# Performance work log

Measured on AMD Instinct MI355X. Metric: run time of the kernel, lower is better.

The kernel has to match this reference:

```python
import jax, jax.numpy as jnp
import numpy as np
from jax import lax

A_RATIOS = (0.5, 1.0, 2.0)
A_SCALES = (8, 16, 32)
FEAT_STRIDE = 16
BASE_SIZE = 16
PRE_NMS = 6000     # n_test_pre_nms
POST_NMS = 300     # n_test_post_nms
NMS_THRESH = 0.7
MIN_SIZE = 16.0
SCALE = 1.0        # forward(scale=1.0) default
NEG = -1e10


def _anchor_base():
    # standard generate_anchor_base: centered at (8,8), ratios x scales
    py = px = BASE_SIZE / 2.0
    rows = []
    for r in A_RATIOS:
        for s in A_SCALES:
            h = BASE_SIZE * s * np.sqrt(r)
            w = BASE_SIZE * s * np.sqrt(1.0 / r)
            rows.append([py - h / 2.0, px - w / 2.0, py + h / 2.0, px + w / 2.0])
    return np.asarray(rows, np.float32)  # (A, 4)


def _all_anchors(height, width):
    base = jnp.asarray(_anchor_base())                                  # (A, 4)
    sy = (jnp.arange(height) * FEAT_STRIDE).astype(jnp.float32)
    sx = (jnp.arange(width) * FEAT_STRIDE).astype(jnp.float32)
    gy, gx = jnp.meshgrid(sy, sx, indexing='ij')
    shift = jnp.stack([gy.ravel(), gx.ravel(), gy.ravel(), gx.ravel()], axis=1)  # (K, 4)
    anch = base[None, :, :] + shift[:, None, :]                         # (K, A, 4)
    return anch.reshape(-1, 4)                                          # (K*A, 4)


def _conv(x, w, b, pad):
    y = lax.conv_general_dilated(x, w, (1, 1), [(pad, pad), (pad, pad)],
                                 dimension_numbers=('NCHW', 'OIHW', 'NCHW'))
    return y + b[None, :, None, None]


def _loc2bbox(anchors, locs):
    h = anchors[:, 2] - anchors[:, 0]
    w = anchors[:, 3] - anchors[:, 1]
    cy = anchors[:, 0] + 0.5 * h
    cx = anchors[:, 1] + 0.5 * w
    dy, dx, dh, dw = locs[:, 0], locs[:, 1], locs[:, 2], locs[:, 3]
    ncy = dy * h + cy
    ncx = dx * w + cx
    nh = jnp.exp(dh) * h
    nw = jnp.exp(dw) * w
    return jnp.stack([ncy - 0.5 * nh, ncx - 0.5 * nw,
                      ncy + 0.5 * nh, ncx + 0.5 * nw], axis=1)


def _iou_one_vs_all(box, boxes):
    ty = jnp.maximum(box[0], boxes[:, 0])
    tx = jnp.maximum(box[1], boxes[:, 1])
    by = jnp.minimum(box[2], boxes[:, 2])
    bx = jnp.minimum(box[3], boxes[:, 3])
    inter = jnp.maximum(by - ty, 0.0) * jnp.maximum(bx - tx, 0.0)
    a1 = (box[2] - box[0]) * (box[3] - box[1])
    a2 = (boxes[:, 2] - boxes[:, 0]) * (boxes[:, 3] - boxes[:, 1])
    return inter / (a1 + a2 - inter + 1e-9)


def _nms(boxes, scores):
    # greedy NMS with fixed POST_NMS output; invalid slots are zero boxes
    def step(s, _):
        i = jnp.argmax(s)
        valid = s[i] > NEG / 2
        ious = _iou_one_vs_all(boxes[i], boxes)
        s = jnp.where(ious > NMS_THRESH, NEG, s)  # suppresses self (iou=1)
        return s, (i, valid)
    _, (idx, valid) = lax.scan(step, scores, None, length=POST_NMS)
    return boxes[idx] * valid[:, None].astype(boxes.dtype)  # (POST_NMS, 4)


def _proposals(anchors, locs, fg, img_h, img_w):
    boxes = _loc2bbox(anchors, locs)
    boxes = jnp.stack([jnp.clip(boxes[:, 0], 0.0, img_h),
                       jnp.clip(boxes[:, 1], 0.0, img_w),
                       jnp.clip(boxes[:, 2], 0.0, img_h),
                       jnp.clip(boxes[:, 3], 0.0, img_w)], axis=1)
    hs = boxes[:, 2] - boxes[:, 0]
    ws = boxes[:, 3] - boxes[:, 1]
    ok = (hs >= MIN_SIZE * SCALE) & (ws >= MIN_SIZE * SCALE)
    sc = jnp.where(ok, fg, NEG)
    top_sc, idx = lax.top_k(sc, PRE_NMS)
    return _nms(boxes[idx], top_sc)


def reference(base_feat, W_conv1, b_conv1, W_score, b_score, W_loc, b_loc, img_h, img_w):
    N, _, H, W = base_feat.shape
    A = 9
    mid = jax.nn.relu(_conv(base_feat, W_conv1, b_conv1, 1))            # (N,512,H,W)
    rpn_locs = _conv(mid, W_loc, b_loc, 0).transpose(0, 2, 3, 1).reshape(N, H * W * A, 4)
    raw = _conv(mid, W_score, b_score, 0).transpose(0, 2, 3, 1)          # (N,H,W,2A)
    rpn_scores = raw.reshape(N, H * W * A, 2)
    fg = jax.nn.softmax(raw.reshape(N, H, W, A, 2), axis=-1)[..., 1].reshape(N, -1)
    anchors = _all_anchors(H, W)                                         # (H*W*A,4)
    ih, iw = float(img_h), float(img_w)
    prop = jax.vmap(lambda l, f: _proposals(anchors, l, f, ih, iw))(rpn_locs, fg)
    rois = prop.reshape(N * POST_NMS, 4)
    roi_indices = jnp.repeat(jnp.arange(N, dtype=jnp.int32), POST_NMS)
    return rpn_locs, rpn_scores, rois, roi_indices, anchors


def setup_inputs() -> dict:
    key = jax.random.key(0)
    k0, k1, k2, k3 = jax.random.split(key, 4)
    N, C, H, W = 4, 512, 64, 64
    nA = 9
    return {
        'base_feat': jax.random.normal(k0, (N, C, H, W), jnp.float32),
        'W_conv1': 0.01 * jax.random.normal(k1, (512, 512, 3, 3), jnp.float32),
        'b_conv1': jnp.zeros((512,), jnp.float32),
        'W_score': 0.01 * jax.random.normal(k2, (2 * nA, 512, 1, 1), jnp.float32),
        'b_score': jnp.zeros((2 * nA,), jnp.float32),
        'W_loc': 0.01 * jax.random.normal(k3, (4 * nA, 512, 1, 1), jnp.float32),
        'b_loc': jnp.zeros((4 * nA,), jnp.float32),
        'img_h': 1024,
        'img_w': 1024,
    }
```

## Files before the change

### kernel.cpp

```cpp
#include <hip/hip_runtime.h>
#include <math.h>

#define HH 64
#define WW 64
#define NIMG 4
#define CIN 512
#define AA 9
#define HWA (HH*WW*AA)
#define PRE_NMS 6000
#define POST_NMS 300
#define NEGV (-1e10f)
#define NEGK 0xD01502F9u
#define NWORD 94

#define OFF1 589824
#define OFF2 884736
#define OFF3 889536
#define OFF4 890736

typedef unsigned int u32;
typedef unsigned long long u64;
typedef _Float16 f16;
typedef _Float16 half8 __attribute__((ext_vector_type(8)));
typedef float f32x4 __attribute__((ext_vector_type(4)));

__device__ __forceinline__ void gload_lds16(const void* g, void* l)
{
    __builtin_amdgcn_global_load_lds((const __attribute__((address_space(1))) void*)g,
                                     (__attribute__((address_space(3))) void*)l,
                                     16, 0, 0);
}

__global__ __launch_bounds__(256) void k_prep_x(const float* __restrict__ x,
                                                f16* __restrict__ xh,
                                                f16* __restrict__ xl)
{
    __shared__ float tile[64][65];
    int ci0 = blockIdx.x * 64, y = blockIdx.y, n = blockIdx.z;
    int t = threadIdx.x;
    #pragma unroll
    for (int l = 0; l < 16; ++l) {
        int idx = l * 256 + t;
        int cc = idx >> 6, xc = idx & 63;
        tile[cc][xc] = x[((size_t)(n * CIN + ci0 + cc) * HH + y) * WW + xc];
    }
    __syncthreads();
    #pragma unroll
    for (int l = 0; l < 16; ++l) {
        int idx = l * 256 + t;
        int xc = idx >> 6, cc = idx & 63;
        float v = tile[cc][xc];
        f16 hi = (f16)v;
        f16 lo = (f16)(v - (float)hi);
        size_t o = ((size_t)(n * 64 + y) * 64 + xc) * 512 + ci0 + cc;
        xh[o] = hi; xl[o] = lo;
    }
}

__global__ __launch_bounds__(256) void k_prep_w(const float* __restrict__ W1,
                                                f16* __restrict__ wh,
                                                f16* __restrict__ wl)
{
    int idx = blockIdx.x * 256 + threadIdx.x;
    int co = idx >> 9, ci = idx & 511;
    #pragma unroll
    for (int tap = 0; tap < 9; ++tap) {
        float v = W1[(size_t)idx * 9 + tap];
        f16 hi = (f16)v;
        f16 lo = (f16)(v - (float)hi);
        size_t o = ((size_t)tap * 512 + co) * 512 + ci;
        wh[o] = hi; wl[o] = lo;
    }
}

__global__ __launch_bounds__(256, 4) void k_conv_mfma(const f16* __restrict__ xh,
                                                      const f16* __restrict__ xl,
                                                      const f16* __restrict__ wh,
                                                      const f16* __restrict__ wl,
                                                      const float* __restrict__ bias,
                                                      float* __restrict__ mid)
{
    __shared__ f16 sX[2][4][64][32];
    const int t = threadIdx.x;
    const int lid = blockIdx.x + 8 * (blockIdx.y + 32 * blockIdx.z);
    const int logical = (lid & 7) * 128 + (lid >> 3);
    const int co0 = (logical & 7) * 64;
    const int g = logical >> 3;
    const int yb = g & 31, n = g >> 5;
    const int y0 = yb * 2;
    const int wv = t >> 6, lane = t & 63;
    const int q = lane >> 4, li = lane & 15;
    const int mh = wv & 1;
    const int xhp = wv >> 1;

    if (yb == 0 || yb == 31) {
        int rowu = (yb == 0) ? 0 : 3072;
        u32* p = (u32*)&sX[0][0][0][0];
        #pragma unroll
        for (int l = 0; l < 8; ++l) {
            int idx = l * 256 + t;
            int plane = idx >> 10, r = idx & 1023;
            p[plane * 4096 + rowu + r] = 0;
        }
    }

    f32x4 acc[2][2][2];
    #pragma unroll
    for (int mt = 0; mt < 2; ++mt)
        #pragma unroll
        for (int xn = 0; xn < 2; ++xn)
            #pragma unroll
            for (int yy = 0; yy < 2; ++yy)
                acc[mt][xn][yy] = (f32x4){0.f, 0.f, 0.f, 0.f};

    auto prefetch = [&](int ci0) {
        #pragma unroll
        for (int m = 0; m < 8; ++m) {
            int k2 = wv * 8 + m;
            int plane = k2 >> 4;
            int row = (k2 >> 2) & 3;
            int gy = y0 - 1 + row;
            if ((unsigned)gy < 64u) {
                int col = ((k2 & 3) << 4) + (lane >> 2);
                int s = (lane & 3) ^ ((lane >> 3) & 3);
                const f16* src = (plane ? xl : xh) +
                    (((size_t)(n * 64 + gy) * 64 + col) * 512 + ci0 + s * 8);
                f16* dst = &sX[0][0][0][0] + (size_t)k2 * 512 + lane * 8;
                gload_lds16(src, dst);
            }
        }
    };

    const size_t wb0 = (size_t)(co0 + mh * 32 + li) * 512 + q * 8;
    const f16* pWh = wh + wb0;
    const f16* pWl = wl + wb0;
    half8 wa[2][2], wn[2][2];
    auto loadW = [&](half8 (&w)[2][2], int ci0, int tap) {
        #pragma unroll
        for (int mt = 0; mt < 2; ++mt) {
            size_t off = (size_t)tap * 262144 + (size_t)mt * 8192 + ci0;
            w[0][mt] = *(const half8*)(pWh + off);
            w[1][mt] = *(const half8*)(pWl + off);
        }
    };

    const f16* pB[2][3];
    bool ob[2][3];
    #pragma unroll
    for (int xn = 0; xn < 2; ++xn)
        #pragma unroll
        for (int kx = 0; kx < 3; ++kx) {
            int xc = xhp * 32 + xn * 16 + li;
            int colr = xc + kx - 1;
            bool o = (colr < 0) || (colr > 63);
            int colc = o ? 0 : colr;
            int qe = q ^ ((colc >> 1) & 3);
            ob[xn][kx] = o;
            pB[xn][kx] = &sX[0][0][colc][qe * 8];
        }

    const half8 zero8 = {(f16)0, (f16)0, (f16)0, (f16)0, (f16)0, (f16)0, (f16)0, (f16)0};

    auto loadB = [&](half8 (&Bf)[2][2][2], int tap) {
        const int ky = tap / 3, kx = tap - ky * 3;
        #pragma unroll
        for (int xn = 0; xn < 2; ++xn) {
            const f16* pb = pB[xn][kx];
            #pragma unroll
            for (int yy = 0; yy < 2; ++yy) {
                const f16* ph = pb + (yy + ky) * 2048;
                half8 vh = *(const half8*)ph;
                half8 vl = *(const half8*)(ph + 8192);
                if (ob[xn][kx]) { vh = zero8; vl = zero8; }
                Bf[0][xn][yy] = vh; Bf[1][xn][yy] = vl;
            }
        }
    };

    prefetch(0);
    loadW(wa, 0, 0);

    for (int chunk = 0; chunk < 16; ++chunk) {
        const int ci0 = chunk * 32;
        __syncthreads();

        half8 B0[2][2][2], Bn[2][2][2];
        loadB(B0, 0);

        #pragma unroll
        for (int tap = 0; tap < 9; ++tap) {
            if (tap < 8) {
                loadW(wn, ci0, tap + 1);
                loadB(Bn, tap + 1);
            }
            #pragma unroll
            for (int mt = 0; mt < 2; ++mt)
                #pragma unroll
                for (int xn = 0; xn < 2; ++xn)
                    #pragma unroll
                    for (int yy = 0; yy < 2; ++yy)
                        acc[mt][xn][yy] = __builtin_amdgcn_mfma_f32_16x16x32_f16(wa[0][mt], B0[0][xn][yy], acc[mt][xn][yy], 0, 0, 0);
            #pragma unroll
            for (int mt = 0; mt < 2; ++mt)
                #pragma unroll
                for (int xn = 0; xn < 2; ++xn)
                    #pragma unroll
                    for (int yy = 0; yy < 2; ++yy)
                        acc[mt][xn][yy] = __builtin_amdgcn_mfma_f32_16x16x32_f16(wa[0][mt], B0[1][xn][yy], acc[mt][xn][yy], 0, 0, 0);
            #pragma unroll
            for (int mt = 0; mt < 2; ++mt)
                #pragma unroll
                for (int xn = 0; xn < 2; ++xn)
                    #pragma unroll
                    for (int yy = 0; yy < 2; ++yy)
                        acc[mt][xn][yy] = __builtin_amdgcn_mfma_f32_16x16x32_f16(wa[1][mt], B0[0][xn][yy], acc[mt][xn][yy], 0, 0, 0);

            if (tap < 8) {
                #pragma unroll
                for (int pl = 0; pl < 2; ++pl)
                    #pragma unroll
                    for (int mt = 0; mt < 2; ++mt) wa[pl][mt] = wn[pl][mt];
                #pragma unroll
                for (int pl = 0; pl < 2; ++pl)
                    #pragma unroll
                    for (int xn = 0; xn < 2; ++xn)
                        #pragma unroll
                        for (int yy = 0; yy < 2; ++yy) B0[pl][xn][yy] = Bn[pl][xn][yy];
            }
        }

        if (chunk + 1 < 16) {
            __syncthreads();
            prefetch(ci0 + 32);
            loadW(wa, ci0 + 32, 0);
        }
    }

    #pragma unroll
    for (int mt = 0; mt < 2; ++mt) {
        #pragma unroll
        for (int r = 0; r < 4; ++r) {
            int co = co0 + mh * 32 + mt * 16 + q * 4 + r;
            float bv = bias[co];
            #pragma unroll
            for (int xn = 0; xn < 2; ++xn) {
                int xc = xhp * 32 + xn * 16 + li;
                #pragma unroll
                for (int yy = 0; yy < 2; ++yy) {
                    float v = acc[mt][xn][yy][r] + bv;
                    mid[((size_t)(n * 512 + co) * HH + y0 + yy) * WW + xc] = v > 0.f ? v : 0.f;
                }
            }
        }
    }
}

__global__ __launch_bounds__(256) void k_htrans(const float* __restrict__ Ws,
                                                const float* __restrict__ Wl,
                                                float* __restrict__ Wt2)
{
    int i = blockIdx.x * 256 + threadIdx.x;
    if (i >= 512 * 64) return;
    int ci = i >> 6, co = i & 63;
    float v = 0.f;
    if (co < 18) v = Ws[co * 512 + ci];
    else if (co < 54) v = Wl[(co - 18) * 512 + ci];
    Wt2[i] = v;
}

__global__ __launch_bounds__(256) void k_hgemm(const float* __restrict__ mid,
                                               const float* __restrict__ Wt2,
                                               float* __restrict__ sraw)
{
    __shared__ float sM[32][64];
    __shared__ float sW2[32][64];
    const int t = threadIdx.x;
    const int px0 = blockIdx.x * 64, n = blockIdx.y;
    const int tx = t & 15, ty = t >> 4;

    float acc[4][4];
    #pragma unroll
    for (int c = 0; c < 4; ++c)
        #pragma unroll
        for (int j = 0; j < 4; ++j) acc[c][j] = 0.f;

    for (int ci0 = 0; ci0 < 512; ci0 += 32) {
        __syncthreads();
        #pragma unroll
        for (int l = 0; l < 8; ++l) {
            int i = l * 256 + t;
            int ci = i >> 6, px = i & 63;
            sM[ci][px] = mid[((size_t)n * 512 + ci0 + ci) * 4096 + px0 + px];
            sW2[ci][px] = Wt2[(size_t)(ci0 + ci) * 64 + px];
        }
        __syncthreads();
        #pragma unroll
        for (int ci = 0; ci < 32; ++ci) {
            float mv[4], wv[4];
            #pragma unroll
            for (int j = 0; j < 4; ++j) mv[j] = sM[ci][tx * 4 + j];
            #pragma unroll
            for (int c = 0; c < 4; ++c) wv[c] = sW2[ci][ty * 4 + c];
            #pragma unroll
            for (int c = 0; c < 4; ++c)
                #pragma unroll
                for (int j = 0; j < 4; ++j) acc[c][j] += wv[c] * mv[j];
        }
    }
    #pragma unroll
    for (int c = 0; c < 4; ++c) {
        float4 v = make_float4(acc[c][0], acc[c][1], acc[c][2], acc[c][3]);
        *(float4*)&sraw[((size_t)n * 64 + ty * 4 + c) * 4096 + px0 + tx * 4] = v;
    }
}

__global__ __launch_bounds__(256) void k_decode(const float* __restrict__ sraw,
                                                const float* __restrict__ bsc,
                                                const float* __restrict__ blc,
                                                const int* __restrict__ ph,
                                                const int* __restrict__ pw,
                                                float* __restrict__ out,
                                                float* __restrict__ boxes,
                                                u32* __restrict__ key)
{
    int p = blockIdx.x * 256 + threadIdx.x;
    int n = p >> 12, pi = p & 4095;
    int y = pi >> 6, xq = pi & 63;

    const float* S = sraw + (size_t)n * 64 * 4096 + pi;
    float* o0 = out + (size_t)n * 147456;
    float* o1 = out + OFF1 + (size_t)n * 73728;
    float IHf = (float)(*ph), IWf = (float)(*pw);

    #pragma unroll
    for (int a = 0; a < 9; ++a) {
        float s0 = S[(size_t)(2 * a) * 4096] + bsc[2 * a];
        float s1 = S[(size_t)(2 * a + 1) * 4096] + bsc[2 * a + 1];
        float dy = S[(size_t)(18 + 4 * a) * 4096] + blc[4 * a];
        float dx = S[(size_t)(19 + 4 * a) * 4096] + blc[4 * a + 1];
        float dh = S[(size_t)(20 + 4 * a) * 4096] + blc[4 * a + 2];
        float dw = S[(size_t)(21 + 4 * a) * 4096] + blc[4 * a + 3];

        o1[(pi * 9 + a) * 2 + 0] = s0;
        o1[(pi * 9 + a) * 2 + 1] = s1;
        o0[(pi * 9 + a) * 4 + 0] = dy;
        o0[(pi * 9 + a) * 4 + 1] = dx;
        o0[(pi * 9 + a) * 4 + 2] = dh;
        o0[(pi * 9 + a) * 4 + 3] = dw;

        float mm = fmaxf(s0, s1);
        float e0 = expf(s0 - mm), e1 = expf(s1 - mm);
        float fg = e1 / (e0 + e1);

        int ri = a / 3, si = a - ri * 3;
        double s = (double)(8 << si);
        double rr = (ri == 0) ? 0.5 : ((ri == 1) ? 1.0 : 2.0);
        double hh = 16.0 * s * sqrt(rr);
        double wd = 16.0 * s * sqrt(1.0 / rr);
        float a0 = (float)(8.0 - hh * 0.5) + (float)(y * 16);
        float a1 = (float)(8.0 - wd * 0.5) + (float)(xq * 16);
        float a2 = (float)(8.0 + hh * 0.5) + (float)(y * 16);
        float a3 = (float)(8.0 + wd * 0.5) + (float)(xq * 16);

        float h = a2 - a0, w = a3 - a1;
        float cy = a0 + 0.5f * h, cx = a1 + 0.5f * w;
        float ncy = dy * h + cy, ncx = dx * w + cx;
        float nh = expf(dh) * h, nw = expf(dw) * w;
        float b0 = fminf(fmaxf(ncy - 0.5f * nh, 0.f), IHf);
        float b1 = fminf(fmaxf(ncx - 0.5f * nw, 0.f), IWf);
        float b2 = fminf(fmaxf(ncy + 0.5f * nh, 0.f), IHf);
        float b3 = fminf(fmaxf(ncx + 0.5f * nw, 0.f), IWf);

        bool ok = (b2 - b0 >= 16.0f) && (b3 - b1 >= 16.0f);
        float sc = ok ? fg : NEGV;

        int gi = n * HWA + pi * 9 + a;
        ((float4*)boxes)[gi] = make_float4(b0, b1, b2, b3);
        u32 u = __float_as_uint(sc);
        u32 kasc = (u & 0x80000000u) ? ~u : (u | 0x80000000u);
        key[gi] = ~kasc;
    }
}

__global__ void k_misc(float* __restrict__ out)
{
    int i = blockIdx.x * 256 + threadIdx.x;
    if (i < 4800) out[OFF2 + i] = 0.f;
    if (i < 1200) out[OFF3 + i] = (float)(i / 300);
    if (i < HWA) {
        int pi = i / 9, a = i - pi * 9;
        int y = pi >> 6, xq = pi & 63;
        int ri = a / 3, si = a - ri * 3;
        double s = (double)(8 << si);
        double rr = (ri == 0) ? 0.5 : ((ri == 1) ? 1.0 : 2.0);
        double hh = 16.0 * s * sqrt(rr);
        double wd = 16.0 * s * sqrt(1.0 / rr);
        out[OFF4 + i * 4 + 0] = (float)(8.0 - hh * 0.5) + (float)(y * 16);
        out[OFF4 + i * 4 + 1] = (float)(8.0 - wd * 0.5) + (float)(xq * 16);
        out[OFF4 + i * 4 + 2] = (float)(8.0 + hh * 0.5) + (float)(y * 16);
        out[OFF4 + i * 4 + 3] = (float)(8.0 + wd * 0.5) + (float)(xq * 16);
    }
}

__global__ __launch_bounds__(1024) void k_select(const u32* __restrict__ key,
                                                 u64* __restrict__ cmp,
                                                 int* __restrict__ nvalid)
{
    __shared__ int hist[256];
    __shared__ u32 sPref;
    __shared__ int sR;
    __shared__ int cLess, cEq, cVal;
    int n = blockIdx.x, t = threadIdx.x;
    const u32* k0 = key + (size_t)n * HWA;

    u32 pref = 0, mask = 0;
    int R = PRE_NMS;
    for (int pass = 0; pass < 4; ++pass) {
        int shift = 24 - pass * 8;
        if (t < 256) hist[t] = 0;
        __syncthreads();
        for (int i = t; i < HWA; i += 1024) {
            u32 k = k0[i];
            if ((k & mask) == pref) atomicAdd(&hist[(k >> shift) & 255], 1);
        }
        __syncthreads();
        if (t == 0) {
            int cum = 0;
            for (int b = 0; b < 256; ++b) {
                int c = hist[b];
                if (cum + c >= R) { sPref = pref | ((u32)b << shift); sR = R - cum; break; }
                cum += c;
            }
        }
        __syncthreads();
        pref = sPref; R = sR; mask |= (0xFFu << shift);
        __syncthreads();
    }
    u32 T = pref;
    if (t == 0) { cLess = 0; cEq = 0; cVal = 0; }
    __syncthreads();
    for (int i = t; i < HWA; i += 1024) {
        u32 k = k0[i];
        if (k < NEGK) atomicAdd(&cVal, 1);
        if (k < T) {
            int p = atomicAdd(&cLess, 1);
            cmp[(size_t)n * 8192 + p] = ((u64)k << 32) | (u32)i;
        } else if (k == T) {
            int p = atomicAdd(&cEq, 1);
            if (p < R) cmp[(size_t)n * 8192 + (PRE_NMS - 1 - p)] = ((u64)k << 32) | (u32)i;
        }
    }
    for (int i = PRE_NMS + t; i < 8192; i += 1024) cmp[(size_t)n * 8192 + i] = ~0ull;
    __syncthreads();
    if (t == 0) nvalid[n] = cVal < PRE_NMS ? cVal : PRE_NMS;
}

__global__ __launch_bounds__(1024) void k_sort(const u64* __restrict__ cmp,
                                               const float* __restrict__ boxes,
                                               float* __restrict__ boxesS)
{
    __shared__ u64 sK[8192];
    int n = blockIdx.x, t = threadIdx.x;
    for (int i = t; i < 8192; i += 1024) sK[i] = cmp[(size_t)n * 8192 + i];
    for (unsigned k = 2; k <= 8192; k <<= 1) {
        for (unsigned j = k >> 1; j > 0; j >>= 1) {
            __syncthreads();
            #pragma unroll
            for (int v = 0; v < 8; ++v) {
                int i = v * 1024 + t;
                int ixj = i ^ (int)j;
                if (ixj > i) {
                    u64 a = sK[i], b = sK[ixj];
                    bool up = ((i & (int)k) == 0);
                    if (up ? (a > b) : (a < b)) { sK[i] = b; sK[ixj] = a; }
                }
            }
        }
    }
    __syncthreads();
    const float4* bsrc = (const float4*)boxes + (size_t)n * HWA;
    float4* bdst = (float4*)boxesS + (size_t)n * PRE_NMS;
    for (int i = t; i < PRE_NMS; i += 1024) {
        u32 idx = (u32)(sK[i] & 0xFFFFFFFFu);
        bdst[i] = bsrc[idx];
    }
}

__global__ __launch_bounds__(64) void k_iou(const float* __restrict__ boxesS,
                                            u64* __restrict__ mask)
{
    __shared__ float4 cb[64];
    int w = blockIdx.x, ic = blockIdx.y, n = blockIdx.z;
    if (w < ic) return;
    int t = threadIdx.x;
    const float4* B = (const float4*)boxesS + (size_t)n * PRE_NMS;
    int jc = w * 64 + t;
    cb[t] = (jc < PRE_NMS) ? B[jc] : make_float4(0.f, 0.f, 0.f, 0.f);
    __syncthreads();
    int i = ic * 64 + t;
    if (i >= PRE_NMS) return;
    float4 bb = B[i];
    float area1 = (bb.z - bb.x) * (bb.w - bb.y);
    u64 m = 0;
    #pragma unroll 8
    for (int j = 0; j < 64; ++j) {
        float4 o = cb[j];
        float ty_ = fmaxf(bb.x, o.x), tx_ = fmaxf(bb.y, o.y);
        float by_ = fminf(bb.z, o.z), bx_ = fminf(bb.w, o.w);
        float inter = fmaxf(by_ - ty_, 0.f) * fmaxf(bx_ - tx_, 0.f);
        float area2 = (o.z - o.x) * (o.w - o.y);
        float iou = inter / (area1 + area2 - inter + 1e-9f);
        if (iou > 0.7f) m |= (1ull << j);
    }
    mask[((size_t)n * PRE_NMS + i) * NWORD + w] = m;
}

__global__ __launch_bounds__(64) void k_nms3(const u64* __restrict__ mask,
                                             const int* __restrict__ nvalid,
                                             const float* __restrict__ boxesS,
                                             float* __restrict__ rois)
{
    int n = blockIdx.x, lane = threadIdx.x;
    int nv = nvalid[n];
    const u64* M = mask + (size_t)n * PRE_NMS * NWORD;
    const float4* B = (const float4*)boxesS + (size_t)n * PRE_NMS;

    auto vmask = [&](int w) -> u64 {
        int lo = w * 64;
        if (nv >= lo + 64) return ~0ull;
        if (nv <= lo) return 0ull;
        return (1ull << (nv - lo)) - 1ull;
    };
    u64 vm0 = vmask(lane);
    u64 vm1 = (lane < NWORD - 64) ? vmask(64 + lane) : 0ull;
    u64 rem0 = 0, rem1 = 0;

    int cnt = 0;
    while (cnt < POST_NMS) {
        u64 c0 = (~rem0) & vm0;
        u64 c1 = (~rem1) & vm1;
        int sel;
        u64 b0 = __ballot(c0 != 0);
        if (b0) {
            int l = __builtin_ctzll(b0);
            u64 w = __shfl(c0, l);
            sel = l * 64 + __builtin_ctzll(w);
        } else {
            u64 b1 = __ballot(c1 != 0);
            if (!b1) break;
            int l = __builtin_ctzll(b1);
            u64 w = __shfl(c1, l);
            sel = (64 + l) * 64 + __builtin_ctzll(w);
        }
        if (lane == 0) {
            float4 bb = B[sel];
            float* orow = rois + (size_t)(n * POST_NMS + cnt) * 4;
            orow[0] = bb.x; orow[1] = bb.y; orow[2] = bb.z; orow[3] = bb.w;
        }
        const u64* Mr = M + (size_t)sel * NWORD;
        rem0 |= Mr[lane];
        if (lane < NWORD - 64) rem1 |= Mr[64 + lane];
        cnt++;
    }
}

extern "C" void kernel_launch(void* const* d_in, const int* in_sizes, int n_in,
                              void* d_out, int out_size, void* d_ws, size_t ws_size,
                              hipStream_t stream)
{
    const float* x  = (const float*)d_in[0];
    const float* W1 = (const float*)d_in[1];
    const float* b1 = (const float*)d_in[2];
    const float* Ws = (const float*)d_in[3];
    const float* bs = (const float*)d_in[4];
    const float* Wl = (const float*)d_in[5];
    const float* bl = (const float*)d_in[6];
    const int* ih   = (const int*)d_in[7];
    const int* iw   = (const int*)d_in[8];
    float* out = (float*)d_out;
    char* ws = (char*)d_ws;

    f16*   Wh2    = (f16*)  (ws);
    f16*   Wl2    = (f16*)  (ws + 4718592);
    float* mid    = (float*)(ws + 9437184);
    f16*   xh     = (f16*)  (ws + 42991616);
    f16*   xl     = (f16*)  (ws + 59768832);
    float* boxes  = (float*)(ws + 42991616);
    u32*   key    = (u32*)  (ws + 45350912);
    u64*   cmp    = (u64*)  (ws + 45940736);
    float* boxesS = (float*)(ws + 46202880);
    int*   nval   = (int*)  (ws + 46586880);
    float* Wt2    = (float*)(ws);
    float* sraw   = (float*)(ws + 262144);
    u64*   iomask = (u64*)  (ws + 9437184);

    k_prep_x<<<dim3(8, 64, 4), 256, 0, stream>>>(x, xh, xl);
    k_prep_w<<<1024, 256, 0, stream>>>(W1, Wh2, Wl2);
    k_conv_mfma<<<dim3(8, 32, 4), 256, 0, stream>>>(xh, xl, Wh2, Wl2, b1, mid);
    k_htrans<<<128, 256, 0, stream>>>(Ws, Wl, Wt2);
    k_hgemm<<<dim3(64, 4), 256, 0, stream>>>(mid, Wt2, sraw);
    k_decode<<<64, 256, 0, stream>>>(sraw, bs, bl, ih, iw, out, boxes, key);
    k_misc<<<144, 256, 0, stream>>>(out);
    k_select<<<4, 1024, 0, stream>>>(key, cmp, nval);
    k_sort<<<4, 1024, 0, stream>>>(cmp, boxes, boxesS);
    k_iou<<<dim3(NWORD, NWORD, NIMG), 64, 0, stream>>>(boxesS, iomask);
    k_nms3<<<NIMG, 64, 0, stream>>>(iomask, nval, boxesS, out + OFF2);
}
```

Before: 846.9 us.

## Double-buffer conv input tiles in LDS to overlap loads with MFMA

Turns the shared-memory input tile for the 3x3 conv into a two-buffer ping-pong. The next channel chunk is prefetched asynchronously into the other buffer while the current one feeds the MFMAs, and partial vmcnt waits with raw barriers replace the full syncthreads pairs. This is meant to hide global-to-LDS latency. In exchange it doubles LDS per block and drops the occupancy hint from 4 to 2 blocks, and the hand-written waitcnt counts must match the number of loads each thread issues.

```diff
diff --git a/kernel.cpp b/kernel.cpp
--- a/kernel.cpp
+++ b/kernel.cpp
@@ -73,14 +73,14 @@
     }
 }
 
-__global__ __launch_bounds__(256, 4) void k_conv_mfma(const f16* __restrict__ xh,
+__global__ __launch_bounds__(256, 2) void k_conv_mfma(const f16* __restrict__ xh,
                                                       const f16* __restrict__ xl,
                                                       const f16* __restrict__ wh,
                                                       const f16* __restrict__ wl,
                                                       const float* __restrict__ bias,
                                                       float* __restrict__ mid)
 {
-    __shared__ f16 sX[2][4][64][32];
+    __shared__ f16 sX[2][2][4][64][32];
     const int t = threadIdx.x;
     const int lid = blockIdx.x + 8 * (blockIdx.y + 32 * blockIdx.z);
     const int logical = (lid & 7) * 128 + (lid >> 3);
@@ -95,12 +95,12 @@
 
     if (yb == 0 || yb == 31) {
         int rowu = (yb == 0) ? 0 : 3072;
-        u32* p = (u32*)&sX[0][0][0][0];
-        #pragma unroll
-        for (int l = 0; l < 8; ++l) {
+        u32* p = (u32*)&sX[0][0][0][0][0];
+        #pragma unroll
+        for (int l = 0; l < 16; ++l) {
             int idx = l * 256 + t;
-            int plane = idx >> 10, r = idx & 1023;
-            p[plane * 4096 + rowu + r] = 0;
+            int buf = idx >> 11, plane = (idx >> 10) & 1, r = idx & 1023;
+            p[buf * 8192 + plane * 4096 + rowu + r] = 0;
         }
     }
 
@@ -113,7 +113,7 @@
             for (int yy = 0; yy < 2; ++yy)
                 acc[mt][xn][yy] = (f32x4){0.f, 0.f, 0.f, 0.f};
 
-    auto prefetch = [&](int ci0) {
+    auto prefetch = [&](int buf, int ci0) {
         #pragma unroll
         for (int m = 0; m < 8; ++m) {
             int k2 = wv * 8 + m;
@@ -125,7 +125,7 @@
                 int s = (lane & 3) ^ ((lane >> 3) & 3);
                 const f16* src = (plane ? xl : xh) +
                     (((size_t)(n * 64 + gy) * 64 + col) * 512 + ci0 + s * 8);
-                f16* dst = &sX[0][0][0][0] + (size_t)k2 * 512 + lane * 8;
+                f16* dst = &sX[0][0][0][0][0] + (size_t)buf * 16384 + (size_t)k2 * 512 + lane * 8;
                 gload_lds16(src, dst);
             }
         }
@@ -156,16 +156,16 @@
             int colc = o ? 0 : colr;
             int qe = q ^ ((colc >> 1) & 3);
             ob[xn][kx] = o;
-            pB[xn][kx] = &sX[0][0][colc][qe * 8];
+            pB[xn][kx] = &sX[0][0][0][colc][qe * 8];
         }
 
     const half8 zero8 = {(f16)0, (f16)0, (f16)0, (f16)0, (f16)0, (f16)0, (f16)0, (f16)0};
 
-    auto loadB = [&](half8 (&Bf)[2][2][2], int tap) {
+    auto loadB = [&](half8 (&Bf)[2][2][2], int tap, int bo) {
         const int ky = tap / 3, kx = tap - ky * 3;
         #pragma unroll
         for (int xn = 0; xn < 2; ++xn) {
-            const f16* pb = pB[xn][kx];
+            const f16* pb = pB[xn][kx] + bo;
             #pragma unroll
             for (int yy = 0; yy < 2; ++yy) {
                 const f16* ph = pb + (yy + ky) * 2048;
@@ -177,21 +177,32 @@
         }
     };
 
-    prefetch(0);
+    prefetch(0, 0);
+    asm volatile("s_waitcnt vmcnt(0) lgkmcnt(0)" ::: "memory");
+    __builtin_amdgcn_s_barrier();
     loadW(wa, 0, 0);
 
     for (int chunk = 0; chunk < 16; ++chunk) {
         const int ci0 = chunk * 32;
-        __syncthreads();
+        const int bo = (chunk & 1) * 16384;
+
+        if (chunk + 1 < 16) {
+            prefetch((chunk + 1) & 1, ci0 + 32);
+            asm volatile("s_waitcnt vmcnt(8)" ::: "memory");
+        } else {
+            asm volatile("s_waitcnt vmcnt(0)" ::: "memory");
+        }
+        __builtin_amdgcn_s_barrier();
+        __builtin_amdgcn_sched_barrier(0);
 
         half8 B0[2][2][2], Bn[2][2][2];
-        loadB(B0, 0);
+        loadB(B0, 0, bo);
 
         #pragma unroll
         for (int tap = 0; tap < 9; ++tap) {
             if (tap < 8) {
                 loadW(wn, ci0, tap + 1);
-                loadB(Bn, tap + 1);
+                loadB(Bn, tap + 1, bo);
             }
             #pragma unroll
             for (int mt = 0; mt < 2; ++mt)
@@ -230,9 +241,8 @@
         }
 
         if (chunk + 1 < 16) {
-            __syncthreads();
-            prefetch(ci0 + 32);
             loadW(wa, ci0 + 32, 0);
+            __builtin_amdgcn_s_barrier();
         }
     }
 
```

Result: no change. 856.8 us (+1.2%).

## Fuse IoU mask and greedy NMS into one LDS-resident kernel

Applied to the files above, without the earlier changes.

Replaces the full pairwise IoU bitmask kernel and the serial mask-scan NMS with a single 1024-thread block per image. The block keeps all 6000 sorted boxes in shared memory and, after each selection, computes IoU of the selected box against every box on the fly. It then clears suppressed candidate bits with ballots. This avoids computing and storing the roughly 36M-entry upper-triangular IoU mask, at the cost of two block barriers per kept box and only 4 active blocks. Anchor base coordinates are also precomputed on the host and passed as a kernel argument instead of being derived with double-precision math in the decode and misc kernels.

```diff
diff --git a/kernel.cpp b/kernel.cpp
--- a/kernel.cpp
+++ b/kernel.cpp
@@ -23,6 +23,8 @@
 typedef _Float16 f16;
 typedef _Float16 half8 __attribute__((ext_vector_type(8)));
 typedef float f32x4 __attribute__((ext_vector_type(4)));
+
+struct AnchBase { float v[36]; };
 
 __device__ __forceinline__ void gload_lds16(const void* g, void* l)
 {
@@ -321,7 +323,8 @@
                                                 const int* __restrict__ pw,
                                                 float* __restrict__ out,
                                                 float* __restrict__ boxes,
-                                                u32* __restrict__ key)
+                                                u32* __restrict__ key,
+                                                AnchBase ab)
 {
     int p = blockIdx.x * 256 + threadIdx.x;
     int n = p >> 12, pi = p & 4095;
@@ -352,15 +355,10 @@
         float e0 = expf(s0 - mm), e1 = expf(s1 - mm);
         float fg = e1 / (e0 + e1);
 
-        int ri = a / 3, si = a - ri * 3;
-        double s = (double)(8 << si);
-        double rr = (ri == 0) ? 0.5 : ((ri == 1) ? 1.0 : 2.0);
-        double hh = 16.0 * s * sqrt(rr);
-        double wd = 16.0 * s * sqrt(1.0 / rr);
-        float a0 = (float)(8.0 - hh * 0.5) + (float)(y * 16);
-        float a1 = (float)(8.0 - wd * 0.5) + (float)(xq * 16);
-        float a2 = (float)(8.0 + hh * 0.5) + (float)(y * 16);
-        float a3 = (float)(8.0 + wd * 0.5) + (float)(xq * 16);
+        float a0 = ab.v[4 * a + 0] + (float)(y * 16);
+        float a1 = ab.v[4 * a + 1] + (float)(xq * 16);
+        float a2 = ab.v[4 * a + 2] + (float)(y * 16);
+        float a3 = ab.v[4 * a + 3] + (float)(xq * 16);
 
         float h = a2 - a0, w = a3 - a1;
         float cy = a0 + 0.5f * h, cx = a1 + 0.5f * w;
@@ -382,7 +380,7 @@
     }
 }
 
-__global__ void k_misc(float* __restrict__ out)
+__global__ void k_misc(float* __restrict__ out, AnchBase ab)
 {
     int i = blockIdx.x * 256 + threadIdx.x;
     if (i < 4800) out[OFF2 + i] = 0.f;
@@ -390,15 +388,10 @@
     if (i < HWA) {
         int pi = i / 9, a = i - pi * 9;
         int y = pi >> 6, xq = pi & 63;
-        int ri = a / 3, si = a - ri * 3;
-        double s = (double)(8 << si);
-        double rr = (ri == 0) ? 0.5 : ((ri == 1) ? 1.0 : 2.0);
-        double hh = 16.0 * s * sqrt(rr);
-        double wd = 16.0 * s * sqrt(1.0 / rr);
-        out[OFF4 + i * 4 + 0] = (float)(8.0 - hh * 0.5) + (float)(y * 16);
-        out[OFF4 + i * 4 + 1] = (float)(8.0 - wd * 0.5) + (float)(xq * 16);
-        out[OFF4 + i * 4 + 2] = (float)(8.0 + hh * 0.5) + (float)(y * 16);
-        out[OFF4 + i * 4 + 3] = (float)(8.0 + wd * 0.5) + (float)(xq * 16);
+        out[OFF4 + i * 4 + 0] = ab.v[4 * a + 0] + (float)(y * 16);
+        out[OFF4 + i * 4 + 1] = ab.v[4 * a + 1] + (float)(xq * 16);
+        out[OFF4 + i * 4 + 2] = ab.v[4 * a + 2] + (float)(y * 16);
+        out[OFF4 + i * 4 + 3] = ab.v[4 * a + 3] + (float)(xq * 16);
     }
 }
 
@@ -486,81 +479,74 @@
     }
 }
 
-__global__ __launch_bounds__(64) void k_iou(const float* __restrict__ boxesS,
-                                            u64* __restrict__ mask)
-{
-    __shared__ float4 cb[64];
-    int w = blockIdx.x, ic = blockIdx.y, n = blockIdx.z;
-    if (w < ic) return;
-    int t = threadIdx.x;
+__global__ __launch_bounds__(1024) void k_nms_fused(const float* __restrict__ boxesS,
+                                                    const int* __restrict__ nvalid,
+                                                    float* __restrict__ rois)
+{
+    __shared__ float4 sB[PRE_NMS];
+    __shared__ u64 cand[NWORD];
+    __shared__ int sSel;
+    const int n = blockIdx.x, t = threadIdx.x;
+    const int wv = t >> 6, lane = t & 63;
+    const int nv = nvalid[n];
+
     const float4* B = (const float4*)boxesS + (size_t)n * PRE_NMS;
-    int jc = w * 64 + t;
-    cb[t] = (jc < PRE_NMS) ? B[jc] : make_float4(0.f, 0.f, 0.f, 0.f);
+    for (int i = t; i < PRE_NMS; i += 1024) sB[i] = B[i];
+    if (t < NWORD) {
+        int lo = t * 64;
+        cand[t] = (nv >= lo + 64) ? ~0ull : (nv <= lo ? 0ull : ((1ull << (nv - lo)) - 1ull));
+    }
     __syncthreads();
-    int i = ic * 64 + t;
-    if (i >= PRE_NMS) return;
-    float4 bb = B[i];
-    float area1 = (bb.z - bb.x) * (bb.w - bb.y);
-    u64 m = 0;
-    #pragma unroll 8
-    for (int j = 0; j < 64; ++j) {
-        float4 o = cb[j];
-        float ty_ = fmaxf(bb.x, o.x), tx_ = fmaxf(bb.y, o.y);
-        float by_ = fminf(bb.z, o.z), bx_ = fminf(bb.w, o.w);
-        float inter = fmaxf(by_ - ty_, 0.f) * fmaxf(bx_ - tx_, 0.f);
-        float area2 = (o.z - o.x) * (o.w - o.y);
-        float iou = inter / (area1 + area2 - inter + 1e-9f);
-        if (iou > 0.7f) m |= (1ull << j);
-    }
-    mask[((size_t)n * PRE_NMS + i) * NWORD + w] = m;
-}
-
-__global__ __launch_bounds__(64) void k_nms3(const u64* __restrict__ mask,
-                                             const int* __restrict__ nvalid,
-                                             const float* __restrict__ boxesS,
-                                             float* __restrict__ rois)
-{
-    int n = blockIdx.x, lane = threadIdx.x;
-    int nv = nvalid[n];
-    const u64* M = mask + (size_t)n * PRE_NMS * NWORD;
-    const float4* B = (const float4*)boxesS + (size_t)n * PRE_NMS;
-
-    auto vmask = [&](int w) -> u64 {
-        int lo = w * 64;
-        if (nv >= lo + 64) return ~0ull;
-        if (nv <= lo) return 0ull;
-        return (1ull << (nv - lo)) - 1ull;
-    };
-    u64 vm0 = vmask(lane);
-    u64 vm1 = (lane < NWORD - 64) ? vmask(64 + lane) : 0ull;
-    u64 rem0 = 0, rem1 = 0;
-
-    int cnt = 0;
-    while (cnt < POST_NMS) {
-        u64 c0 = (~rem0) & vm0;
-        u64 c1 = (~rem1) & vm1;
-        int sel;
-        u64 b0 = __ballot(c0 != 0);
-        if (b0) {
-            int l = __builtin_ctzll(b0);
-            u64 w = __shfl(c0, l);
-            sel = l * 64 + __builtin_ctzll(w);
-        } else {
-            u64 b1 = __ballot(c1 != 0);
-            if (!b1) break;
-            int l = __builtin_ctzll(b1);
-            u64 w = __shfl(c1, l);
-            sel = (64 + l) * 64 + __builtin_ctzll(w);
-        }
-        if (lane == 0) {
-            float4 bb = B[sel];
+
+    for (int cnt = 0; cnt < POST_NMS; ++cnt) {
+        if (wv == 0) {
+            u64 w0 = (lane < NWORD) ? cand[lane] : 0ull;
+            u64 w1 = (lane < NWORD - 64) ? cand[64 + lane] : 0ull;
+            int sel = -1;
+            u64 b0 = __ballot(w0 != 0);
+            if (b0) {
+                int l = __builtin_ctzll(b0);
+                u64 w = __shfl(w0, l);
+                sel = l * 64 + __builtin_ctzll(w);
+            } else {
+                u64 b1 = __ballot(w1 != 0);
+                if (b1) {
+                    int l = __builtin_ctzll(b1);
+                    u64 w = __shfl(w1, l);
+                    sel = (64 + l) * 64 + __builtin_ctzll(w);
+                }
+            }
+            if (lane == 0) sSel = sel;
+        }
+        __syncthreads();
+        int sel = sSel;
+        if (sel < 0) break;
+
+        float4 bb = sB[sel];
+        if (t == 0) {
             float* orow = rois + (size_t)(n * POST_NMS + cnt) * 4;
             orow[0] = bb.x; orow[1] = bb.y; orow[2] = bb.z; orow[3] = bb.w;
         }
-        const u64* Mr = M + (size_t)sel * NWORD;
-        rem0 |= Mr[lane];
-        if (lane < NWORD - 64) rem1 |= Mr[64 + lane];
-        cnt++;
+        float area1 = (bb.z - bb.x) * (bb.w - bb.y);
+
+        #pragma unroll
+        for (int k = 0; k < 6; ++k) {
+            int j = k * 1024 + t;
+            bool supp = false;
+            if (j < PRE_NMS) {
+                float4 o = sB[j];
+                float ty_ = fmaxf(bb.x, o.x), tx_ = fmaxf(bb.y, o.y);
+                float by_ = fminf(bb.z, o.z), bx_ = fminf(bb.w, o.w);
+                float inter = fmaxf(by_ - ty_, 0.f) * fmaxf(bx_ - tx_, 0.f);
+                float area2 = (o.z - o.x) * (o.w - o.y);
+                float iou = inter / (area1 + area2 - inter + 1e-9f);
+                supp = iou > 0.7f;
+            }
+            u64 bm = __ballot(supp);
+            int w = k * 16 + wv;
+            if (lane == 0 && w < NWORD && bm) cand[w] &= ~bm;
+        }
+        __syncthreads();
     }
 }
 
@@ -592,17 +578,28 @@
     int*   nval   = (int*)  (ws + 46586880);
     float* Wt2    = (float*)(ws);
     float* sraw   = (float*)(ws + 262144);
-    u64*   iomask = (u64*)  (ws + 9437184);
+
+    AnchBase ab;
+    for (int a = 0; a < 9; ++a) {
+        int ri = a / 3, si = a - ri * 3;
+        double s = (double)(8 << si);
+        double rr = (ri == 0) ? 0.5 : ((ri == 1) ? 1.0 : 2.0);
+        double hh = 16.0 * s * sqrt(rr);
+        double wd = 16.0 * s * sqrt(1.0 / rr);
+        ab.v[a * 4 + 0] = (float)(8.0 - hh * 0.5);
+        ab.v[a * 4 + 1] = (float)(8.0 - wd * 0.5);
+        ab.v[a * 4 + 2] = (float)(8.0 + hh * 0.5);
+        ab.v[a * 4 + 3] = (float)(8.0 + wd * 0.5);
+    }
 
     k_prep_x<<<dim3(8, 64, 4), 256, 0, stream>>>(x, xh, xl);
     k_prep_w<<<1024, 256, 0, stream>>>(W1, Wh2, Wl2);
     k_conv_mfma<<<dim3(8, 32, 4), 256, 0, stream>>>(xh, xl, Wh2, Wl2, b1, mid);
     k_htrans<<<128, 256, 0, stream>>>(Ws, Wl, Wt2);
     k_hgemm<<<dim3(64, 4), 256, 0, stream>>>(mid, Wt2, sraw);
-    k_decode<<<64, 256, 0, stream>>>(sraw, bs, bl, ih, iw, out, boxes, key);
-    k_misc<<<144, 256, 0, stream>>>(out);
+    k_decode<<<64, 256, 0, stream>>>(sraw, bs, bl, ih, iw, out, boxes, key, ab);
+    k_misc<<<144, 256, 0, stream>>>(out, ab);
     k_select<<<4, 1024, 0, stream>>>(key, cmp, nval);
     k_sort<<<4, 1024, 0, stream>>>(cmp, boxes, boxesS);
-    k_iou<<<dim3(NWORD, NWORD, NIMG), 64, 0, stream>>>(boxesS, iomask);
-    k_nms3<<<NIMG, 64, 0, stream>>>(iomask, nval, boxesS, out + OFF2);
-}
+    k_nms_fused<<<NIMG, 1024, 0, stream>>>(boxesS, nval, out + OFF2);
+}
```

After: 1.104 ms. 1.3x slower.
